# Kernel tuning notes

Measured on AMD Instinct MI355X. Metric: run time of the kernel, lower is better.

The kernel has to match this reference:

```python
import jax, jax.numpy as jnp
import numpy as np

EPS = 1e-10


def setup_inputs() -> dict:
    key = jax.random.key(0)
    k1, k2, k3 = jax.random.split(key, 3)
    B, X, Y = 16, 512, 512
    predictions = jax.random.uniform(k1, (B, 5, X, Y), dtype=jnp.float32)
    inputs = jax.random.uniform(k2, (B, 3, X, Y), dtype=jnp.float32)
    heart = jax.random.randint(k3, (B, 1, X, Y), 0, 2, dtype=jnp.int32)
    return {"predictions": predictions, "inputs": inputs, "heart": heart}


def reference(predictions, inputs, heart):
    # predictions: [B,5,X,Y] soft class maps (chan 0 unused); inputs: [B,3,X,Y] MRI modalities
    # heart: [B,1,X,Y] binary ROI mask. Loops over b/k/m in the torch source are vectorized;
    # boolean-mask gathers become multiply-by-mask with masked reductions (same math).
    mask = (heart[:, 0] == 1).astype(predictions.dtype)          # [B,X,Y]
    pred = predictions[:, 1:5]                                   # [B,K=4,X,Y]
    inp = inputs                                                 # [B,M=3,X,Y]

    w = pred * mask[:, None]                                     # masked soft weights [B,K,X,Y]
    sw = jnp.sum(w, axis=(2, 3))                                 # [B,K]
    denom = sw[:, :, None] + EPS                                 # [B,K,1]

    # per-(k,m) weighted mean over masked pixels
    mu = jnp.einsum('bkxy,bmxy->bkm', w, inp) / denom            # [B,K,M]
    diff = inp[:, None, :, :, :] - mu[:, :, :, None, None]       # [B,K,M,X,Y]
    var = jnp.einsum('bkxy,bkmxy->bkm', w, diff * diff) / denom + EPS

    # Gaussian pdf per (k,m,pixel), scaled by pred_k (as in temp[k,m] = pred[k]*pdf)
    inv_norm = 1.0 / jnp.sqrt(2.0 * jnp.pi * var)                # [B,K,M]
    pdf = inv_norm[:, :, :, None, None] * jnp.exp(
        -(diff * diff) / (2.0 * var)[:, :, :, None, None])      # [B,K,M,X,Y]
    temp = pred[:, :, None] * pdf                                # [B,K,M,X,Y]

    mix = jnp.sum(jnp.prod(temp, axis=2), axis=1)                # [B,X,Y]
    loglik = jnp.log(mix + EPS)                                  # [B,X,Y]

    # masked mean over ROI pixels per batch (== torch.mean over gathered pixels)
    per_b = -jnp.sum(loglik * mask, axis=(1, 2)) / jnp.sum(mask, axis=(1, 2))
    return jnp.mean(per_b)
```

## Files before the change

### kernel.cpp

```cpp
#include <hip/hip_runtime.h>
#include <math.h>

constexpr int NB = 16;
constexpr int XY = 512 * 512;
constexpr int NV = XY / 4;
constexpr int WS_STRIDE = 32;


__device__ __forceinline__ float waveReduce64(float v) {
#pragma unroll
    for (int off = 32; off > 0; off >>= 1) v += __shfl_down(v, off, 64);
    return v;
}

#define PIX1(h_, e0_, e1_, e2_, p0_, p1_, p2_, p3_) do {                      \
    float mm_ = ((h_) == 1) ? 1.f : 0.f;                                      \
    cnt += mm_;                                                               \
    float w0_ = (p0_) * mm_, w1_ = (p1_) * mm_, w2_ = (p2_) * mm_,            \
          w3_ = (p3_) * mm_;                                                  \
    s0_0 += w0_; s0_1 += w1_; s0_2 += w2_; s0_3 += w3_;                       \
    float t_;                                                                 \
    t_ = w0_ * (e0_); u00 += t_; q00 = fmaf(t_, (e0_), q00);                  \
    t_ = w0_ * (e1_); u01 += t_; q01 = fmaf(t_, (e1_), q01);                  \
    t_ = w0_ * (e2_); u02 += t_; q02 = fmaf(t_, (e2_), q02);                  \
    t_ = w1_ * (e0_); u10 += t_; q10 = fmaf(t_, (e0_), q10);                  \
    t_ = w1_ * (e1_); u11 += t_; q11 = fmaf(t_, (e1_), q11);                  \
    t_ = w1_ * (e2_); u12 += t_; q12 = fmaf(t_, (e2_), q12);                  \
    t_ = w2_ * (e0_); u20 += t_; q20 = fmaf(t_, (e0_), q20);                  \
    t_ = w2_ * (e1_); u21 += t_; q21 = fmaf(t_, (e1_), q21);                  \
    t_ = w2_ * (e2_); u22 += t_; q22 = fmaf(t_, (e2_), q22);                  \
    t_ = w3_ * (e0_); u30 += t_; q30 = fmaf(t_, (e0_), q30);                  \
    t_ = w3_ * (e1_); u31 += t_; q31 = fmaf(t_, (e1_), q31);                  \
    t_ = w3_ * (e2_); u32 += t_; q32 = fmaf(t_, (e2_), q32);                  \
} while (0)

#define RED(i_, var_) { float r_ = waveReduce64(var_); if (lane == 0) sh[wav][i_] = r_; }

__global__ __launch_bounds__(256) void pass1_moments(
        const float* __restrict__ predictions,
        const float* __restrict__ inputs,
        const int*   __restrict__ heart,
        double*      __restrict__ ws) {
    const int b = blockIdx.y;
    const float4* P1 = reinterpret_cast<const float4*>(predictions + (size_t)b * 5 * XY + 1 * XY);
    const float4* P2 = reinterpret_cast<const float4*>(predictions + (size_t)b * 5 * XY + 2 * XY);
    const float4* P3 = reinterpret_cast<const float4*>(predictions + (size_t)b * 5 * XY + 3 * XY);
    const float4* P4 = reinterpret_cast<const float4*>(predictions + (size_t)b * 5 * XY + 4 * XY);
    const float4* I0 = reinterpret_cast<const float4*>(inputs + (size_t)b * 3 * XY + 0 * XY);
    const float4* I1 = reinterpret_cast<const float4*>(inputs + (size_t)b * 3 * XY + 1 * XY);
    const float4* I2 = reinterpret_cast<const float4*>(inputs + (size_t)b * 3 * XY + 2 * XY);
    const int4*   H  = reinterpret_cast<const int4*>(heart + (size_t)b * XY);

    float cnt = 0.f;
    float s0_0 = 0.f, s0_1 = 0.f, s0_2 = 0.f, s0_3 = 0.f;
    float u00 = 0.f, u01 = 0.f, u02 = 0.f, u10 = 0.f, u11 = 0.f, u12 = 0.f;
    float u20 = 0.f, u21 = 0.f, u22 = 0.f, u30 = 0.f, u31 = 0.f, u32 = 0.f;
    float q00 = 0.f, q01 = 0.f, q02 = 0.f, q10 = 0.f, q11 = 0.f, q12 = 0.f;
    float q20 = 0.f, q21 = 0.f, q22 = 0.f, q30 = 0.f, q31 = 0.f, q32 = 0.f;

    const int tid0   = blockIdx.x * blockDim.x + threadIdx.x;
    const int stride = gridDim.x * blockDim.x;

    for (int v = tid0; v < NV; v += stride) {
        int4   h  = H[v];
        float4 f0 = I0[v], f1 = I1[v], f2 = I2[v];
        float4 g0 = P1[v], g1 = P2[v], g2 = P3[v], g3 = P4[v];
        PIX1(h.x, f0.x, f1.x, f2.x, g0.x, g1.x, g2.x, g3.x);
        PIX1(h.y, f0.y, f1.y, f2.y, g0.y, g1.y, g2.y, g3.y);
        PIX1(h.z, f0.z, f1.z, f2.z, g0.z, g1.z, g2.z, g3.z);
        PIX1(h.w, f0.w, f1.w, f2.w, g0.w, g1.w, g2.w, g3.w);
    }

    __shared__ float sh[4][29];
    const int lane = threadIdx.x & 63;
    const int wav  = threadIdx.x >> 6;
    RED(0, cnt);
    RED(1, s0_0); RED(2, s0_1); RED(3, s0_2); RED(4, s0_3);
    RED(5, u00); RED(6, u01); RED(7, u02);
    RED(8, u10); RED(9, u11); RED(10, u12);
    RED(11, u20); RED(12, u21); RED(13, u22);
    RED(14, u30); RED(15, u31); RED(16, u32);
    RED(17, q00); RED(18, q01); RED(19, q02);
    RED(20, q10); RED(21, q11); RED(22, q12);
    RED(23, q20); RED(24, q21); RED(25, q22);
    RED(26, q30); RED(27, q31); RED(28, q32);
    __syncthreads();
    if (threadIdx.x < 29) {
        float v = sh[0][threadIdx.x] + sh[1][threadIdx.x] + sh[2][threadIdx.x] + sh[3][threadIdx.x];
        atomicAdd(&ws[(size_t)b * WS_STRIDE + threadIdx.x], (double)v);
    }
}

#define PARAMK(K_, mu0_, mu1_, mu2_, h0_, h1_, h2_, C_) {                     \
    double S0_ = w[1 + (K_)];                                                 \
    double den_ = S0_ + 1e-10;                                                \
    double Cd_ = 1.0;                                                         \
    double S1_, S2_, muv_, var_;                                              \
    S1_ = w[5 + (K_)*3 + 0]; S2_ = w[17 + (K_)*3 + 0];                        \
    muv_ = S1_ / den_;                                                        \
    var_ = (S2_ - 2.0 * muv_ * S1_ + muv_ * muv_ * S0_) / den_ + 1e-10;       \
    mu0_ = (float)muv_; h0_ = (float)(0.5 / var_);                            \
    Cd_ *= 1.0 / sqrt(6.283185307179586 * var_);                              \
    S1_ = w[5 + (K_)*3 + 1]; S2_ = w[17 + (K_)*3 + 1];                        \
    muv_ = S1_ / den_;                                                        \
    var_ = (S2_ - 2.0 * muv_ * S1_ + muv_ * muv_ * S0_) / den_ + 1e-10;       \
    mu1_ = (float)muv_; h1_ = (float)(0.5 / var_);                            \
    Cd_ *= 1.0 / sqrt(6.283185307179586 * var_);                              \
    S1_ = w[5 + (K_)*3 + 2]; S2_ = w[17 + (K_)*3 + 2];                        \
    muv_ = S1_ / den_;                                                        \
    var_ = (S2_ - 2.0 * muv_ * S1_ + muv_ * muv_ * S0_) / den_ + 1e-10;       \
    mu2_ = (float)muv_; h2_ = (float)(0.5 / var_);                            \
    Cd_ *= 1.0 / sqrt(6.283185307179586 * var_);                              \
    C_ = (float)Cd_;                                                          \
}

#define PIX2(h_, e0_, e1_, e2_, p0_, p1_, p2_, p3_) do {                      \
    float m_ = ((h_) == 1) ? 1.f : 0.f;                                       \
    float d0_, d1_, d2_, ex_, pc_;                                            \
    float mix_;                                                               \
    d0_ = (e0_) - mu00; d1_ = (e1_) - mu01; d2_ = (e2_) - mu02;               \
    ex_ = fmaf(d0_ * d0_, hv00, fmaf(d1_ * d1_, hv01, d2_ * d2_ * hv02));     \
    pc_ = (p0_) * (p0_) * (p0_);                                              \
    mix_ = C0 * pc_ * __expf(-ex_);                                           \
    d0_ = (e0_) - mu10; d1_ = (e1_) - mu11; d2_ = (e2_) - mu12;               \
    ex_ = fmaf(d0_ * d0_, hv10, fmaf(d1_ * d1_, hv11, d2_ * d2_ * hv12));     \
    pc_ = (p1_) * (p1_) * (p1_);                                              \
    mix_ = fmaf(C1 * pc_, __expf(-ex_), mix_);                                \
    d0_ = (e0_) - mu20; d1_ = (e1_) - mu21; d2_ = (e2_) - mu22;               \
    ex_ = fmaf(d0_ * d0_, hv20, fmaf(d1_ * d1_, hv21, d2_ * d2_ * hv22));     \
    pc_ = (p2_) * (p2_) * (p2_);                                              \
    mix_ = fmaf(C2 * pc_, __expf(-ex_), mix_);                                \
    d0_ = (e0_) - mu30; d1_ = (e1_) - mu31; d2_ = (e2_) - mu32;               \
    ex_ = fmaf(d0_ * d0_, hv30, fmaf(d1_ * d1_, hv31, d2_ * d2_ * hv32));     \
    pc_ = (p3_) * (p3_) * (p3_);                                              \
    mix_ = fmaf(C3 * pc_, __expf(-ex_), mix_);                                \
    lacc += m_ * __logf(mix_ + 1e-10f);                                       \
} while (0)

__global__ __launch_bounds__(256) void pass2_loglik(
        const float* __restrict__ predictions,
        const float* __restrict__ inputs,
        const int*   __restrict__ heart,
        double*      __restrict__ ws) {
    const int b = blockIdx.y;
    const double* w = ws + (size_t)b * WS_STRIDE;

    float mu00, mu01, mu02, mu10, mu11, mu12, mu20, mu21, mu22, mu30, mu31, mu32;
    float hv00, hv01, hv02, hv10, hv11, hv12, hv20, hv21, hv22, hv30, hv31, hv32;
    float C0, C1, C2, C3;
    PARAMK(0, mu00, mu01, mu02, hv00, hv01, hv02, C0);
    PARAMK(1, mu10, mu11, mu12, hv10, hv11, hv12, C1);
    PARAMK(2, mu20, mu21, mu22, hv20, hv21, hv22, C2);
    PARAMK(3, mu30, mu31, mu32, hv30, hv31, hv32, C3);

    const float4* P1 = reinterpret_cast<const float4*>(predictions + (size_t)b * 5 * XY + 1 * XY);
    const float4* P2 = reinterpret_cast<const float4*>(predictions + (size_t)b * 5 * XY + 2 * XY);
    const float4* P3 = reinterpret_cast<const float4*>(predictions + (size_t)b * 5 * XY + 3 * XY);
    const float4* P4 = reinterpret_cast<const float4*>(predictions + (size_t)b * 5 * XY + 4 * XY);
    const float4* I0 = reinterpret_cast<const float4*>(inputs + (size_t)b * 3 * XY + 0 * XY);
    const float4* I1 = reinterpret_cast<const float4*>(inputs + (size_t)b * 3 * XY + 1 * XY);
    const float4* I2 = reinterpret_cast<const float4*>(inputs + (size_t)b * 3 * XY + 2 * XY);
    const int4*   H  = reinterpret_cast<const int4*>(heart + (size_t)b * XY);

    float lacc = 0.f;
    const int tid0   = blockIdx.x * blockDim.x + threadIdx.x;
    const int stride = gridDim.x * blockDim.x;

    for (int v = tid0; v < NV; v += stride) {
        int4   h  = H[v];
        float4 f0 = I0[v], f1 = I1[v], f2 = I2[v];
        float4 g0 = P1[v], g1 = P2[v], g2 = P3[v], g3 = P4[v];
        PIX2(h.x, f0.x, f1.x, f2.x, g0.x, g1.x, g2.x, g3.x);
        PIX2(h.y, f0.y, f1.y, f2.y, g0.y, g1.y, g2.y, g3.y);
        PIX2(h.z, f0.z, f1.z, f2.z, g0.z, g1.z, g2.z, g3.z);
        PIX2(h.w, f0.w, f1.w, f2.w, g0.w, g1.w, g2.w, g3.w);
    }

    __shared__ float sh[4];
    const int lane = threadIdx.x & 63;
    const int wav  = threadIdx.x >> 6;
    float v = waveReduce64(lacc);
    if (lane == 0) sh[wav] = v;
    __syncthreads();
    if (threadIdx.x == 0) {
        float t = sh[0] + sh[1] + sh[2] + sh[3];
        atomicAdd(&ws[(size_t)b * WS_STRIDE + 29], (double)t);
    }
}

__global__ void finalize_kernel(const double* __restrict__ ws, float* __restrict__ out) {
    const int lane = threadIdx.x;
    double v = 0.0;
    if (lane < NB) {
        double cntv = ws[(size_t)lane * WS_STRIDE + 0];
        double ll   = ws[(size_t)lane * WS_STRIDE + 29];
        v = -ll / cntv;
    }
#pragma unroll
    for (int off = 8; off > 0; off >>= 1) v += __shfl_down(v, off, 64);
    if (lane == 0) out[0] = (float)(v / (double)NB);
}

extern "C" void kernel_launch(void* const* d_in, const int* in_sizes, int n_in,
                              void* d_out, int out_size, void* d_ws, size_t ws_size,
                              hipStream_t stream) {
    const float* predictions = (const float*)d_in[0];
    const float* inputs      = (const float*)d_in[1];
    const int*   heart       = (const int*)d_in[2];
    float*  out = (float*)d_out;
    double* ws  = (double*)d_ws;

    hipMemsetAsync(d_ws, 0, (size_t)NB * WS_STRIDE * sizeof(double), stream);

    pass1_moments<<<dim3(64, NB), 256, 0, stream>>>(predictions, inputs, heart, ws);
    pass2_loglik <<<dim3(64, NB), 256, 0, stream>>>(predictions, inputs, heart, ws);
    finalize_kernel<<<1, 64, 0, stream>>>(ws, out);
}
```

Baseline: 194.6 us.

## Drop memset and finalize launch; use per-block partials and last-block finalize

Pass 1 now writes per-block float partial moments to workspace instead of double atomics, and zeroes the pass-2 accumulators itself, so the memset launch goes away. Pass 2 re-reduces the 128 partials per batch in every block, broadcasts the parameters through readfirstlane, and finalizes through arrival counters with a last-block pattern, removing the finalize kernel. The grid doubles to 128 blocks per batch with a fully unrolled fixed-trip loop. The cost is redundant partial reads in every pass-2 block and more complex synchronization that relies on the workspace state left by pass 1.

```diff
diff --git a/kernel.cpp b/kernel.cpp
--- a/kernel.cpp
+++ b/kernel.cpp
@@ -4,13 +4,18 @@
 constexpr int NB = 16;
 constexpr int XY = 512 * 512;
 constexpr int NV = XY / 4;
-constexpr int WS_STRIDE = 32;
-
+constexpr int G  = 128;
+
+constexpr int P1OFF = 512;
 
 __device__ __forceinline__ float waveReduce64(float v) {
 #pragma unroll
     for (int off = 32; off > 0; off >>= 1) v += __shfl_down(v, off, 64);
     return v;
+}
+
+__device__ __forceinline__ float rfl(float x) {
+    return __uint_as_float(__builtin_amdgcn_readfirstlane(__float_as_uint(x)));
 }
 
 #define PIX1(h_, e0_, e1_, e2_, p0_, p1_, p2_, p3_) do {                      \
@@ -36,77 +41,22 @@
 
 #define RED(i_, var_) { float r_ = waveReduce64(var_); if (lane == 0) sh[wav][i_] = r_; }
 
-__global__ __launch_bounds__(256) void pass1_moments(
-        const float* __restrict__ predictions,
-        const float* __restrict__ inputs,
-        const int*   __restrict__ heart,
-        double*      __restrict__ ws) {
-    const int b = blockIdx.y;
-    const float4* P1 = reinterpret_cast<const float4*>(predictions + (size_t)b * 5 * XY + 1 * XY);
-    const float4* P2 = reinterpret_cast<const float4*>(predictions + (size_t)b * 5 * XY + 2 * XY);
-    const float4* P3 = reinterpret_cast<const float4*>(predictions + (size_t)b * 5 * XY + 3 * XY);
-    const float4* P4 = reinterpret_cast<const float4*>(predictions + (size_t)b * 5 * XY + 4 * XY);
-    const float4* I0 = reinterpret_cast<const float4*>(inputs + (size_t)b * 3 * XY + 0 * XY);
-    const float4* I1 = reinterpret_cast<const float4*>(inputs + (size_t)b * 3 * XY + 1 * XY);
-    const float4* I2 = reinterpret_cast<const float4*>(inputs + (size_t)b * 3 * XY + 2 * XY);
-    const int4*   H  = reinterpret_cast<const int4*>(heart + (size_t)b * XY);
-
-    float cnt = 0.f;
-    float s0_0 = 0.f, s0_1 = 0.f, s0_2 = 0.f, s0_3 = 0.f;
-    float u00 = 0.f, u01 = 0.f, u02 = 0.f, u10 = 0.f, u11 = 0.f, u12 = 0.f;
-    float u20 = 0.f, u21 = 0.f, u22 = 0.f, u30 = 0.f, u31 = 0.f, u32 = 0.f;
-    float q00 = 0.f, q01 = 0.f, q02 = 0.f, q10 = 0.f, q11 = 0.f, q12 = 0.f;
-    float q20 = 0.f, q21 = 0.f, q22 = 0.f, q30 = 0.f, q31 = 0.f, q32 = 0.f;
-
-    const int tid0   = blockIdx.x * blockDim.x + threadIdx.x;
-    const int stride = gridDim.x * blockDim.x;
-
-    for (int v = tid0; v < NV; v += stride) {
-        int4   h  = H[v];
-        float4 f0 = I0[v], f1 = I1[v], f2 = I2[v];
-        float4 g0 = P1[v], g1 = P2[v], g2 = P3[v], g3 = P4[v];
-        PIX1(h.x, f0.x, f1.x, f2.x, g0.x, g1.x, g2.x, g3.x);
-        PIX1(h.y, f0.y, f1.y, f2.y, g0.y, g1.y, g2.y, g3.y);
-        PIX1(h.z, f0.z, f1.z, f2.z, g0.z, g1.z, g2.z, g3.z);
-        PIX1(h.w, f0.w, f1.w, f2.w, g0.w, g1.w, g2.w, g3.w);
-    }
-
-    __shared__ float sh[4][29];
-    const int lane = threadIdx.x & 63;
-    const int wav  = threadIdx.x >> 6;
-    RED(0, cnt);
-    RED(1, s0_0); RED(2, s0_1); RED(3, s0_2); RED(4, s0_3);
-    RED(5, u00); RED(6, u01); RED(7, u02);
-    RED(8, u10); RED(9, u11); RED(10, u12);
-    RED(11, u20); RED(12, u21); RED(13, u22);
-    RED(14, u30); RED(15, u31); RED(16, u32);
-    RED(17, q00); RED(18, q01); RED(19, q02);
-    RED(20, q10); RED(21, q11); RED(22, q12);
-    RED(23, q20); RED(24, q21); RED(25, q22);
-    RED(26, q30); RED(27, q31); RED(28, q32);
-    __syncthreads();
-    if (threadIdx.x < 29) {
-        float v = sh[0][threadIdx.x] + sh[1][threadIdx.x] + sh[2][threadIdx.x] + sh[3][threadIdx.x];
-        atomicAdd(&ws[(size_t)b * WS_STRIDE + threadIdx.x], (double)v);
-    }
-}
-
 #define PARAMK(K_, mu0_, mu1_, mu2_, h0_, h1_, h2_, C_) {                     \
-    double S0_ = w[1 + (K_)];                                                 \
+    double S0_ = tot[1 + (K_)];                                               \
     double den_ = S0_ + 1e-10;                                                \
     double Cd_ = 1.0;                                                         \
     double S1_, S2_, muv_, var_;                                              \
-    S1_ = w[5 + (K_)*3 + 0]; S2_ = w[17 + (K_)*3 + 0];                        \
+    S1_ = tot[5 + (K_)*3 + 0]; S2_ = tot[17 + (K_)*3 + 0];                    \
     muv_ = S1_ / den_;                                                        \
     var_ = (S2_ - 2.0 * muv_ * S1_ + muv_ * muv_ * S0_) / den_ + 1e-10;       \
     mu0_ = (float)muv_; h0_ = (float)(0.5 / var_);                            \
     Cd_ *= 1.0 / sqrt(6.283185307179586 * var_);                              \
-    S1_ = w[5 + (K_)*3 + 1]; S2_ = w[17 + (K_)*3 + 1];                        \
+    S1_ = tot[5 + (K_)*3 + 1]; S2_ = tot[17 + (K_)*3 + 1];                    \
     muv_ = S1_ / den_;                                                        \
     var_ = (S2_ - 2.0 * muv_ * S1_ + muv_ * muv_ * S0_) / den_ + 1e-10;       \
     mu1_ = (float)muv_; h1_ = (float)(0.5 / var_);                            \
     Cd_ *= 1.0 / sqrt(6.283185307179586 * var_);                              \
-    S1_ = w[5 + (K_)*3 + 2]; S2_ = w[17 + (K_)*3 + 2];                        \
+    S1_ = tot[5 + (K_)*3 + 2]; S2_ = tot[17 + (K_)*3 + 2];                    \
     muv_ = S1_ / den_;                                                        \
     var_ = (S2_ - 2.0 * muv_ * S1_ + muv_ * muv_ * S0_) / den_ + 1e-10;       \
     mu2_ = (float)muv_; h2_ = (float)(0.5 / var_);                            \
@@ -137,21 +87,14 @@
     lacc += m_ * __logf(mix_ + 1e-10f);                                       \
 } while (0)
 
-__global__ __launch_bounds__(256) void pass2_loglik(
+__global__ __launch_bounds__(256) void pass1_moments(
         const float* __restrict__ predictions,
         const float* __restrict__ inputs,
         const int*   __restrict__ heart,
-        double*      __restrict__ ws) {
-    const int b = blockIdx.y;
-    const double* w = ws + (size_t)b * WS_STRIDE;
-
-    float mu00, mu01, mu02, mu10, mu11, mu12, mu20, mu21, mu22, mu30, mu31, mu32;
-    float hv00, hv01, hv02, hv10, hv11, hv12, hv20, hv21, hv22, hv30, hv31, hv32;
-    float C0, C1, C2, C3;
-    PARAMK(0, mu00, mu01, mu02, hv00, hv01, hv02, C0);
-    PARAMK(1, mu10, mu11, mu12, hv10, hv11, hv12, C1);
-    PARAMK(2, mu20, mu21, mu22, hv20, hv21, hv22, C2);
-    PARAMK(3, mu30, mu31, mu32, hv30, hv31, hv32, C3);
+        char*        __restrict__ wsraw) {
+    const int b   = blockIdx.y;
+    const int g   = blockIdx.x;
+    const int tid = threadIdx.x;
 
     const float4* P1 = reinterpret_cast<const float4*>(predictions + (size_t)b * 5 * XY + 1 * XY);
     const float4* P2 = reinterpret_cast<const float4*>(predictions + (size_t)b * 5 * XY + 2 * XY);
@@ -162,11 +105,115 @@
     const float4* I2 = reinterpret_cast<const float4*>(inputs + (size_t)b * 3 * XY + 2 * XY);
     const int4*   H  = reinterpret_cast<const int4*>(heart + (size_t)b * XY);
 
+    float cnt = 0.f;
+    float s0_0 = 0.f, s0_1 = 0.f, s0_2 = 0.f, s0_3 = 0.f;
+    float u00 = 0.f, u01 = 0.f, u02 = 0.f, u10 = 0.f, u11 = 0.f, u12 = 0.f;
+    float u20 = 0.f, u21 = 0.f, u22 = 0.f, u30 = 0.f, u31 = 0.f, u32 = 0.f;
+    float q00 = 0.f, q01 = 0.f, q02 = 0.f, q10 = 0.f, q11 = 0.f, q12 = 0.f;
+    float q20 = 0.f, q21 = 0.f, q22 = 0.f, q30 = 0.f, q31 = 0.f, q32 = 0.f;
+
+    const int base0 = g * 256 + tid;
+    constexpr int STRIDE = G * 256;
+    constexpr int NIT = NV / STRIDE;
+
+#pragma unroll
+    for (int it = 0; it < NIT; ++it) {
+        const int v = base0 + it * STRIDE;
+        int4   h  = H[v];
+        float4 f0 = I0[v], f1 = I1[v], f2 = I2[v];
+        float4 g0 = P1[v], g1 = P2[v], g2 = P3[v], g3 = P4[v];
+        PIX1(h.x, f0.x, f1.x, f2.x, g0.x, g1.x, g2.x, g3.x);
+        PIX1(h.y, f0.y, f1.y, f2.y, g0.y, g1.y, g2.y, g3.y);
+        PIX1(h.z, f0.z, f1.z, f2.z, g0.z, g1.z, g2.z, g3.z);
+        PIX1(h.w, f0.w, f1.w, f2.w, g0.w, g1.w, g2.w, g3.w);
+    }
+
+    __shared__ float sh[4][29];
+    const int lane = tid & 63;
+    const int wav  = tid >> 6;
+    RED(0, cnt);
+    RED(1, s0_0); RED(2, s0_1); RED(3, s0_2); RED(4, s0_3);
+    RED(5, u00); RED(6, u01); RED(7, u02);
+    RED(8, u10); RED(9, u11); RED(10, u12);
+    RED(11, u20); RED(12, u21); RED(13, u22);
+    RED(14, u30); RED(15, u31); RED(16, u32);
+    RED(17, q00); RED(18, q01); RED(19, q02);
+    RED(20, q10); RED(21, q11); RED(22, q12);
+    RED(23, q20); RED(24, q21); RED(25, q22);
+    RED(26, q30); RED(27, q31); RED(28, q32);
+    __syncthreads();
+
+    float* p1 = reinterpret_cast<float*>(wsraw + P1OFF);
+    if (tid < 29) {
+        float v = sh[0][tid] + sh[1][tid] + sh[2][tid] + sh[3][tid];
+        p1[(((size_t)b * G + g) << 5) + tid] = v;
+    }
+
+    if (b == 0 && g == 0) {
+        double* wsd = reinterpret_cast<double*>(wsraw);
+        if (tid < 17) wsd[tid] = 0.0;
+        int* wsi = reinterpret_cast<int*>(wsd + 17);
+        if (tid >= 32 && tid < 49) wsi[tid - 32] = 0;
+    }
+}
+
+__global__ __launch_bounds__(256) void pass2_loglik(
+        const float* __restrict__ predictions,
+        const float* __restrict__ inputs,
+        const int*   __restrict__ heart,
+        float*       __restrict__ out,
+        char*        __restrict__ wsraw) {
+    const int b   = blockIdx.y;
+    const int g   = blockIdx.x;
+    const int tid = threadIdx.x;
+
+    __shared__ double tot[29];
+    {
+        const float* p1 = reinterpret_cast<const float*>(wsraw + P1OFF);
+        if (tid < 29) {
+            const float* basep = p1 + ((size_t)b * G << 5) + tid;
+            double s = 0.0;
+#pragma unroll 8
+            for (int j = 0; j < G; ++j) s += (double)basep[(size_t)j << 5];
+            tot[tid] = s;
+        }
+    }
+    __syncthreads();
+
+    float mu00, mu01, mu02, mu10, mu11, mu12, mu20, mu21, mu22, mu30, mu31, mu32;
+    float hv00, hv01, hv02, hv10, hv11, hv12, hv20, hv21, hv22, hv30, hv31, hv32;
+    float C0, C1, C2, C3;
+    PARAMK(0, mu00, mu01, mu02, hv00, hv01, hv02, C0);
+    PARAMK(1, mu10, mu11, mu12, hv10, hv11, hv12, C1);
+    PARAMK(2, mu20, mu21, mu22, hv20, hv21, hv22, C2);
+    PARAMK(3, mu30, mu31, mu32, hv30, hv31, hv32, C3);
+    mu00=rfl(mu00); mu01=rfl(mu01); mu02=rfl(mu02);
+    mu10=rfl(mu10); mu11=rfl(mu11); mu12=rfl(mu12);
+    mu20=rfl(mu20); mu21=rfl(mu21); mu22=rfl(mu22);
+    mu30=rfl(mu30); mu31=rfl(mu31); mu32=rfl(mu32);
+    hv00=rfl(hv00); hv01=rfl(hv01); hv02=rfl(hv02);
+    hv10=rfl(hv10); hv11=rfl(hv11); hv12=rfl(hv12);
+    hv20=rfl(hv20); hv21=rfl(hv21); hv22=rfl(hv22);
+    hv30=rfl(hv30); hv31=rfl(hv31); hv32=rfl(hv32);
+    C0=rfl(C0); C1=rfl(C1); C2=rfl(C2); C3=rfl(C3);
+
+    const float4* P1 = reinterpret_cast<const float4*>(predictions + (size_t)b * 5 * XY + 1 * XY);
+    const float4* P2 = reinterpret_cast<const float4*>(predictions + (size_t)b * 5 * XY + 2 * XY);
+    const float4* P3 = reinterpret_cast<const float4*>(predictions + (size_t)b * 5 * XY + 3 * XY);
+    const float4* P4 = reinterpret_cast<const float4*>(predictions + (size_t)b * 5 * XY + 4 * XY);
+    const float4* I0 = reinterpret_cast<const float4*>(inputs + (size_t)b * 3 * XY + 0 * XY);
+    const float4* I1 = reinterpret_cast<const float4*>(inputs + (size_t)b * 3 * XY + 1 * XY);
+    const float4* I2 = reinterpret_cast<const float4*>(inputs + (size_t)b * 3 * XY + 2 * XY);
+    const int4*   H  = reinterpret_cast<const int4*>(heart + (size_t)b * XY);
+
     float lacc = 0.f;
-    const int tid0   = blockIdx.x * blockDim.x + threadIdx.x;
-    const int stride = gridDim.x * blockDim.x;
-
-    for (int v = tid0; v < NV; v += stride) {
+    const int base0 = g * 256 + tid;
+    constexpr int STRIDE = G * 256;
+    constexpr int NIT = NV / STRIDE;
+
+#pragma unroll
+    for (int it = 0; it < NIT; ++it) {
+        const int v = base0 + it * STRIDE;
         int4   h  = H[v];
         float4 f0 = I0[v], f1 = I1[v], f2 = I2[v];
         float4 g0 = P1[v], g1 = P2[v], g2 = P3[v], g3 = P4[v];
@@ -176,29 +223,37 @@
         PIX2(h.w, f0.w, f1.w, f2.w, g0.w, g1.w, g2.w, g3.w);
     }
 
-    __shared__ float sh[4];
-    const int lane = threadIdx.x & 63;
-    const int wav  = threadIdx.x >> 6;
-    float v = waveReduce64(lacc);
-    if (lane == 0) sh[wav] = v;
+    __shared__ float sh2[4];
+    const int lane = tid & 63;
+    const int wav  = tid >> 6;
+    {
+        float v = waveReduce64(lacc);
+        if (lane == 0) sh2[wav] = v;
+    }
     __syncthreads();
-    if (threadIdx.x == 0) {
-        float t = sh[0] + sh[1] + sh[2] + sh[3];
-        atomicAdd(&ws[(size_t)b * WS_STRIDE + 29], (double)t);
-    }
-}
-
-__global__ void finalize_kernel(const double* __restrict__ ws, float* __restrict__ out) {
-    const int lane = threadIdx.x;
-    double v = 0.0;
-    if (lane < NB) {
-        double cntv = ws[(size_t)lane * WS_STRIDE + 0];
-        double ll   = ws[(size_t)lane * WS_STRIDE + 29];
-        v = -ll / cntv;
-    }
-#pragma unroll
-    for (int off = 8; off > 0; off >>= 1) v += __shfl_down(v, off, 64);
-    if (lane == 0) out[0] = (float)(v / (double)NB);
+
+    if (tid == 0) {
+        double* llsum        = reinterpret_cast<double*>(wsraw);
+        double* final_sum    = llsum + 16;
+        int*    arrive       = reinterpret_cast<int*>(llsum + 17);
+        int*    batches_done = arrive + 16;
+
+        float t = sh2[0] + sh2[1] + sh2[2] + sh2[3];
+        atomicAdd(&llsum[b], (double)t);
+        __threadfence();
+        int prev = atomicAdd(&arrive[b], 1);
+        if (prev == G - 1) {
+            double ll  = atomicAdd(&llsum[b], 0.0);
+            double bval = -ll / tot[0];
+            atomicAdd(final_sum, bval * (1.0 / (double)NB));
+            __threadfence();
+            int bprev = atomicAdd(batches_done, 1);
+            if (bprev == NB - 1) {
+                double fs = atomicAdd(final_sum, 0.0);
+                out[0] = (float)fs;
+            }
+        }
+    }
 }
 
 extern "C" void kernel_launch(void* const* d_in, const int* in_sizes, int n_in,
@@ -207,12 +262,9 @@
     const float* predictions = (const float*)d_in[0];
     const float* inputs      = (const float*)d_in[1];
     const int*   heart       = (const int*)d_in[2];
-    float*  out = (float*)d_out;
-    double* ws  = (double*)d_ws;
-
-    hipMemsetAsync(d_ws, 0, (size_t)NB * WS_STRIDE * sizeof(double), stream);
-
-    pass1_moments<<<dim3(64, NB), 256, 0, stream>>>(predictions, inputs, heart, ws);
-    pass2_loglik <<<dim3(64, NB), 256, 0, stream>>>(predictions, inputs, heart, ws);
-    finalize_kernel<<<1, 64, 0, stream>>>(ws, out);
-}
+    float* out   = (float*)d_out;
+    char*  wsraw = (char*)d_ws;
+
+    pass1_moments<<<dim3(G, NB), 256, 0, stream>>>(predictions, inputs, heart, wsraw);
+    pass2_loglik <<<dim3(G, NB), 256, 0, stream>>>(predictions, inputs, heart, out, wsraw);
+}
```

New measurement: 255.2 us. +31.1%, slower.
